# Performance work log

Measured on AMD Instinct MI355X. Metric: run time of the kernel, lower is better.

Reference implementation:

```python
import jax, jax.numpy as jnp
import numpy as np

HEADS = 12
HEAD_SIZE = 64
NEG_BIG = 1e12


def _rope_sin_cos(seq_len, head_size, dtype):
    # embeddings[n, 2i] = sin(n * 10000^(-2i/d)), [n, 2i+1] = cos(...)
    pos = jnp.arange(seq_len, dtype=dtype)                      # [s]
    idx = jnp.arange(head_size // 2, dtype=dtype)               # [d/2]
    inv_freq = jnp.power(jnp.asarray(10000.0, dtype), -2.0 * idx / head_size)
    ang = jnp.einsum('n,d->nd', pos, inv_freq)                  # [s, d/2]
    # cos_pos / sin_pos: repeat_interleave each frequency twice -> [1, s, 1, d]
    cos = jnp.repeat(jnp.cos(ang), 2, axis=-1)[None, :, None, :]
    sin = jnp.repeat(jnp.sin(ang), 2, axis=-1)[None, :, None, :]
    return sin, cos


def _rotate_half_interleaved(x):
    # stack([-x[..., 1::2], x[..., ::2]], -1).reshape_as(x)
    x2 = jnp.stack([-x[..., 1::2], x[..., ::2]], axis=-1)
    return x2.reshape(x.shape)


def setup_inputs() -> dict:
    key = jax.random.key(0)
    k1, k2 = jax.random.split(key)
    bs, s, h = 16, 512, 768
    hidden = jax.random.normal(k1, (bs, s, h), dtype=jnp.float32)
    attention_mask = jnp.ones((bs, s), dtype=jnp.int32)
    W = jax.random.normal(k2, (h, HEADS * 2 * HEAD_SIZE), dtype=jnp.float32) * (h ** -0.5)
    b = jnp.zeros((HEADS * 2 * HEAD_SIZE,), dtype=jnp.float32)
    return {"hidden": hidden, "attention_mask": attention_mask, "W": W, "b": b}


def reference(hidden, attention_mask, W, b):
    bs, s, _ = hidden.shape
    x = hidden @ W + b                                           # [b, s, heads*2*hd]
    x = x.reshape(bs, s, HEADS, 2, HEAD_SIZE)
    qw, kw = x[..., 0, :], x[..., 1, :]                          # [b, s, h, d]

    sin, cos = _rope_sin_cos(s, HEAD_SIZE, hidden.dtype)
    qw = qw * cos + _rotate_half_interleaved(qw) * sin
    kw = kw * cos + _rotate_half_interleaved(kw) * sin

    logits = jnp.einsum('bmhd,bnhd->bhmn', qw, kw)               # [b, h, s, s]

    am = attention_mask.astype(logits.dtype)
    pad_mask = 1.0 - am[:, None, None, :] * am[:, None, :, None]
    logits = logits - pad_mask * NEG_BIG

    tril = jnp.tril(jnp.ones((s, s), dtype=logits.dtype), k=-1)  # strictly lower
    logits = logits - tril[None, None, :, :] * NEG_BIG

    return logits / (HEAD_SIZE ** 0.5)
```

## Files before the change

### kernel.cpp

```cpp
#include <hip/hip_runtime.h>
#include <math.h>

#define HEADS 12
#define HSZ   64
#define SEQ   512
#define BATCH 16
#define HID   768
#define NOUT  1536
#define NEGQ  1.25e11f

typedef _Float16 f16x8 __attribute__((ext_vector_type(8)));
typedef _Float16 f16x4 __attribute__((ext_vector_type(4)));
typedef float    f32x4 __attribute__((ext_vector_type(4)));

__device__ __forceinline__ void async_ld16(const void* g, void* l) {
  __builtin_amdgcn_global_load_lds(
      (__attribute__((address_space(1))) void*)g,
      (__attribute__((address_space(3))) void*)l, 16, 0, 0);
}

__global__ __launch_bounds__(256) void prep_k(
    const float* __restrict__ hidden, const float* __restrict__ W,
    _Float16* __restrict__ Xb, _Float16* __restrict__ Wt,
    float2* __restrict__ tab)
{
  __shared__ float t_lds[32][33];
  const int b = blockIdx.x;
  const int t = threadIdx.x;
  if (b < 1152) {
    const int tk = b % 24, tn = b / 24;
    const int k0 = tk * 32, n0 = tn * 32;
    const int tx = t & 31, ty = t >> 5;
#pragma unroll
    for (int r = 0; r < 4; ++r)
      t_lds[ty + r * 8][tx] = W[(size_t)(k0 + ty + r * 8) * NOUT + n0 + tx];
    __syncthreads();
#pragma unroll
    for (int r = 0; r < 4; ++r)
      Wt[(size_t)(n0 + ty + r * 8) * HID + k0 + tx] = (_Float16)t_lds[tx][ty + r * 8];
  } else if (b < 1152 + 6144) {
    const int idx = (b - 1152) * 256 + t;
    float4 v = ((const float4*)hidden)[idx];
    f16x4 o;
    o.x = (_Float16)v.x; o.y = (_Float16)v.y;
    o.z = (_Float16)v.z; o.w = (_Float16)v.w;
    ((f16x4*)Xb)[idx] = o;
  } else {
    const int e = (b - 7296) * 256 + t;
    const int si = e >> 5, fi = e & 31;
    float inv = powf(10000.f, -(float)fi / 32.f);
    float ang = (float)si * inv;
    float sv, cv;
    sincosf(ang, &sv, &cv);
    tab[e] = make_float2(cv, sv);
  }
}

__global__ __launch_bounds__(256) void gemm1_k(
    const _Float16* __restrict__ Xb, const _Float16* __restrict__ Wt,
    const float* __restrict__ bias, const float2* __restrict__ tab,
    _Float16* __restrict__ qb, _Float16* __restrict__ kb)
{
  __shared__ __align__(16) _Float16 As[128 * 32];
  __shared__ __align__(16) _Float16 Bs[128 * 32];
  const int tid = threadIdx.x;
  const int lane = tid & 63;
  const int m0 = blockIdx.x * 128;
  const int n0 = blockIdx.y * 128;
  const int wm = ((tid >> 6) & 1) * 64;
  const int wn = (tid >> 7) * 64;

  const int s0r = tid >> 2, s0c = (tid & 3) * 8;
  const int s1r = (tid + 256) >> 2;
  const _Float16* ag0 = Xb + (size_t)(m0 + s0r) * HID + s0c;
  const _Float16* ag1 = Xb + (size_t)(m0 + s1r) * HID + s0c;
  const _Float16* bg0 = Wt + (size_t)(n0 + s0r) * HID + s0c;
  const _Float16* bg1 = Wt + (size_t)(n0 + s1r) * HID + s0c;
  _Float16* al0 = &As[tid * 8];
  _Float16* al1 = &As[(tid + 256) * 8];
  _Float16* bl0 = &Bs[tid * 8];
  _Float16* bl1 = &Bs[(tid + 256) * 8];

  const int lrow = lane & 15;
  const int lk = (lane >> 4) * 8;

  f32x4 acc[4][4] = {};

  for (int kt = 0; kt < 24; ++kt) {
    async_ld16(ag0, al0);
    async_ld16(ag1, al1);
    async_ld16(bg0, bl0);
    async_ld16(bg1, bl1);
    ag0 += 32; ag1 += 32; bg0 += 32; bg1 += 32;
    __syncthreads();
    f16x8 af[4], bf[4];
#pragma unroll
    for (int i = 0; i < 4; ++i) {
      af[i] = *(const f16x8*)&As[(wm + i * 16 + lrow) * 32 + lk];
      bf[i] = *(const f16x8*)&Bs[(wn + i * 16 + lrow) * 32 + lk];
    }
#pragma unroll
    for (int i = 0; i < 4; ++i)
#pragma unroll
      for (int j = 0; j < 4; ++j)
        acc[i][j] = __builtin_amdgcn_mfma_f32_16x16x32_f16(bf[j], af[i], acc[i][j], 0, 0, 0);
    __syncthreads();
  }

  const int qlane = lane >> 4;
  const int mlane = m0 + wm + (lane & 15);
#pragma unroll
  for (int j = 0; j < 4; ++j) {
    const int nb = n0 + wn + j * 16 + qlane * 4;
    const float4 b4 = *(const float4*)&bias[nb];
    const int d0 = nb & 63;
    const int h = nb >> 7;
    _Float16* dst = ((nb >> 6) & 1) ? kb : qb;
    const int fi0 = d0 >> 1;
#pragma unroll
    for (int i = 0; i < 4; ++i) {
      const int m = mlane + i * 16;
      const int si = m & (SEQ - 1);
      const int bb = m >> 9;
      const float4 cs = *(const float4*)&tab[si * 32 + fi0];
      const float v0 = acc[i][j][0] + b4.x;
      const float v1 = acc[i][j][1] + b4.y;
      const float v2 = acc[i][j][2] + b4.z;
      const float v3 = acc[i][j][3] + b4.w;
      f16x4 o;
      o.x = (_Float16)fmaf(v0, cs.x, -v1 * cs.y);
      o.y = (_Float16)fmaf(v1, cs.x, v0 * cs.y);
      o.z = (_Float16)fmaf(v2, cs.z, -v3 * cs.w);
      o.w = (_Float16)fmaf(v3, cs.z, v2 * cs.w);
      *(f16x4*)&dst[((size_t)(bb * HEADS + h) * SEQ + si) * HSZ + d0] = o;
    }
  }
}

__global__ __launch_bounds__(256) void gemm2_k(
    const _Float16* __restrict__ qb, const _Float16* __restrict__ kb,
    const int* __restrict__ am, float* __restrict__ out)
{
  __shared__ __align__(16) _Float16 Qs[2 * 128 * 32];
  __shared__ __align__(16) _Float16 Ks[2 * 128 * 32];
  const int tid = threadIdx.x;
  const int bh = blockIdx.y;
  const int bb = bh / HEADS;
  const int mt = blockIdx.x >> 2, nt = blockIdx.x & 3;
  const int m0 = mt * 128, n0 = nt * 128;
  const int* amb = am + bb * SEQ;
  float* obase = out + (size_t)bh * SEQ * SEQ;

  if (nt < mt) {
#pragma unroll
    for (int q = 0; q < 16; ++q) {
      const int f = q * 256 + tid;
      const int row = f >> 5, c4 = (f & 31) * 4;
      const int m = m0 + row;
      const float amm = (float)amb[m];
      const int nb = n0 + c4;
      const int4 a4 = *(const int4*)&amb[nb];
      float4 v;
      v.x = -(2.f - amm * (float)a4.x) * NEGQ;
      v.y = -(2.f - amm * (float)a4.y) * NEGQ;
      v.z = -(2.f - amm * (float)a4.z) * NEGQ;
      v.w = -(2.f - amm * (float)a4.w) * NEGQ;
      *(float4*)&obase[(size_t)m * SEQ + nb] = v;
    }
    return;
  }

  const _Float16* qg = qb + (size_t)bh * SEQ * HSZ;
  const _Float16* kg = kb + (size_t)bh * SEQ * HSZ;
#pragma unroll
  for (int ct = 0; ct < 4; ++ct) {
    const int s = ct * 256 + tid;
    const int half = s >> 9, row = (s >> 2) & 127, c8 = (s & 3) * 8;
    async_ld16(qg + (size_t)(m0 + row) * HSZ + half * 32 + c8, &Qs[s * 8]);
    async_ld16(kg + (size_t)(n0 + row) * HSZ + half * 32 + c8, &Ks[s * 8]);
  }
  __syncthreads();

  const int lane = tid & 63;
  const int wm = ((tid >> 6) & 1) * 64;
  const int wn = (tid >> 7) * 64;
  const int lrow = lane & 15;
  const int lk = (lane >> 4) * 8;
  f32x4 acc[4][4] = {};
#pragma unroll
  for (int half = 0; half < 2; ++half) {
    f16x8 af[4], bf[4];
#pragma unroll
    for (int i = 0; i < 4; ++i) {
      af[i] = *(const f16x8*)&Qs[half * 4096 + (wm + i * 16 + lrow) * 32 + lk];
      bf[i] = *(const f16x8*)&Ks[half * 4096 + (wn + i * 16 + lrow) * 32 + lk];
    }
#pragma unroll
    for (int i = 0; i < 4; ++i)
#pragma unroll
      for (int j = 0; j < 4; ++j)
        acc[i][j] = __builtin_amdgcn_mfma_f32_16x16x32_f16(bf[j], af[i], acc[i][j], 0, 0, 0);
  }

  const int qlane = lane >> 4;
  const int mlane = m0 + wm + (lane & 15);
#pragma unroll
  for (int i = 0; i < 4; ++i) {
    const int m = mlane + i * 16;
    const float amm = (float)amb[m];
    float* orow = obase + (size_t)m * SEQ;
#pragma unroll
    for (int j = 0; j < 4; ++j) {
      const int nb = n0 + wn + j * 16 + qlane * 4;
      const int4 a4 = *(const int4*)&amb[nb];
      float4 v;
      v.x = fmaf(acc[i][j][0], 0.125f,
                 -((float)(nb + 0 < m) + (1.f - amm * (float)a4.x)) * NEGQ);
      v.y = fmaf(acc[i][j][1], 0.125f,
                 -((float)(nb + 1 < m) + (1.f - amm * (float)a4.y)) * NEGQ);
      v.z = fmaf(acc[i][j][2], 0.125f,
                 -((float)(nb + 2 < m) + (1.f - amm * (float)a4.z)) * NEGQ);
      v.w = fmaf(acc[i][j][3], 0.125f,
                 -((float)(nb + 3 < m) + (1.f - amm * (float)a4.w)) * NEGQ);
      *(float4*)&orow[nb] = v;
    }
  }
}

extern "C" void kernel_launch(void* const* d_in, const int* in_sizes, int n_in,
                              void* d_out, int out_size, void* d_ws, size_t ws_size,
                              hipStream_t stream) {
  const float* hidden = (const float*)d_in[0];
  const int*   am     = (const int*)d_in[1];
  const float* W      = (const float*)d_in[2];
  const float* bias   = (const float*)d_in[3];
  float* out = (float*)d_out;
  char* ws = (char*)d_ws;
  _Float16* Xb = (_Float16*)(ws);
  _Float16* Wt = (_Float16*)(ws + 12582912);
  _Float16* qb = (_Float16*)(ws + 14942208);
  _Float16* kb = (_Float16*)(ws + 27525120);
  float2*   tab = (float2*)(ws + 40108032);

  prep_k<<<dim3(7360), dim3(256), 0, stream>>>(hidden, W, Xb, Wt, tab);
  gemm1_k<<<dim3(64, 12), dim3(256), 0, stream>>>(Xb, Wt, bias, tab, qb, kb);
  gemm2_k<<<dim3(16, 192), dim3(256), 0, stream>>>(qb, kb, am, out);
}
```

Before: 306.7 us.

## Quantize projection GEMM inputs to FP8 and use scaled MFMA with swizzled LDS

The hidden-state and weight conversion now packs values to FP8 instead of FP16. The first GEMM runs on the 16x16x128 FP8 scaled MFMA with 128-wide K tiles and an XOR-swizzled LDS layout, cutting conversion traffic and the number of K iterations. The Q·K kernel now loads operands straight from global memory into registers, and output stores become nontemporal. FP8 input precision loosens accuracy of the logits, which may push error tolerances.

After: 274.8 us. 1.12x faster.

```diff
diff --git a/kernel.cpp b/kernel.cpp
--- a/kernel.cpp
+++ b/kernel.cpp
@@ -4,7 +4,6 @@
 #define HEADS 12
 #define HSZ   64
 #define SEQ   512
-#define BATCH 16
 #define HID   768
 #define NOUT  1536
 #define NEGQ  1.25e11f
@@ -12,6 +11,8 @@
 typedef _Float16 f16x8 __attribute__((ext_vector_type(8)));
 typedef _Float16 f16x4 __attribute__((ext_vector_type(4)));
 typedef float    f32x4 __attribute__((ext_vector_type(4)));
+typedef int      i32x4 __attribute__((ext_vector_type(4)));
+typedef int      i32x8 __attribute__((ext_vector_type(8)));
 
 __device__ __forceinline__ void async_ld16(const void* g, void* l) {
   __builtin_amdgcn_global_load_lds(
@@ -21,7 +22,7 @@
 
 __global__ __launch_bounds__(256) void prep_k(
     const float* __restrict__ hidden, const float* __restrict__ W,
-    _Float16* __restrict__ Xb, _Float16* __restrict__ Wt,
+    unsigned char* __restrict__ Xb8, unsigned char* __restrict__ Wt8,
     float2* __restrict__ tab)
 {
   __shared__ float t_lds[32][33];
@@ -35,18 +36,28 @@
     for (int r = 0; r < 4; ++r)
       t_lds[ty + r * 8][tx] = W[(size_t)(k0 + ty + r * 8) * NOUT + n0 + tx];
     __syncthreads();
-#pragma unroll
-    for (int r = 0; r < 4; ++r)
-      Wt[(size_t)(n0 + ty + r * 8) * HID + k0 + tx] = (_Float16)t_lds[tx][ty + r * 8];
-  } else if (b < 1152 + 6144) {
+    const int nl = t >> 3, kg = t & 7;
+    int w = __builtin_amdgcn_cvt_pk_fp8_f32(t_lds[kg * 4 + 0][nl],
+                                            t_lds[kg * 4 + 1][nl], 0, false);
+    w = __builtin_amdgcn_cvt_pk_fp8_f32(t_lds[kg * 4 + 2][nl],
+                                        t_lds[kg * 4 + 3][nl], w, true);
+    *(int*)&Wt8[(size_t)(n0 + nl) * HID + k0 + kg * 4] = w;
+  } else if (b < 1152 + 1536) {
     const int idx = (b - 1152) * 256 + t;
-    float4 v = ((const float4*)hidden)[idx];
-    f16x4 o;
-    o.x = (_Float16)v.x; o.y = (_Float16)v.y;
-    o.z = (_Float16)v.z; o.w = (_Float16)v.w;
-    ((f16x4*)Xb)[idx] = o;
+    const float4* src = (const float4*)hidden + (size_t)idx * 4;
+    float4 v0 = src[0], v1 = src[1], v2 = src[2], v3 = src[3];
+    int4 o;
+    o.x = __builtin_amdgcn_cvt_pk_fp8_f32(v0.x, v0.y, 0, false);
+    o.x = __builtin_amdgcn_cvt_pk_fp8_f32(v0.z, v0.w, o.x, true);
+    o.y = __builtin_amdgcn_cvt_pk_fp8_f32(v1.x, v1.y, 0, false);
+    o.y = __builtin_amdgcn_cvt_pk_fp8_f32(v1.z, v1.w, o.y, true);
+    o.z = __builtin_amdgcn_cvt_pk_fp8_f32(v2.x, v2.y, 0, false);
+    o.z = __builtin_amdgcn_cvt_pk_fp8_f32(v2.z, v2.w, o.z, true);
+    o.w = __builtin_amdgcn_cvt_pk_fp8_f32(v3.x, v3.y, 0, false);
+    o.w = __builtin_amdgcn_cvt_pk_fp8_f32(v3.z, v3.w, o.w, true);
+    ((int4*)Xb8)[idx] = o;
   } else {
-    const int e = (b - 7296) * 256 + t;
+    const int e = (b - 2688) * 256 + t;
     const int si = e >> 5, fi = e & 31;
     float inv = powf(10000.f, -(float)fi / 32.f);
     float ang = (float)si * inv;
@@ -57,53 +68,55 @@
 }
 
 __global__ __launch_bounds__(256) void gemm1_k(
-    const _Float16* __restrict__ Xb, const _Float16* __restrict__ Wt,
+    const unsigned char* __restrict__ Xb8, const unsigned char* __restrict__ Wt8,
     const float* __restrict__ bias, const float2* __restrict__ tab,
     _Float16* __restrict__ qb, _Float16* __restrict__ kb)
 {
-  __shared__ __align__(16) _Float16 As[128 * 32];
-  __shared__ __align__(16) _Float16 Bs[128 * 32];
+  __shared__ __align__(16) int As4[4096];
+  __shared__ __align__(16) int Bs4[4096];
   const int tid = threadIdx.x;
   const int lane = tid & 63;
   const int m0 = blockIdx.x * 128;
   const int n0 = blockIdx.y * 128;
   const int wm = ((tid >> 6) & 1) * 64;
   const int wn = (tid >> 7) * 64;
-
-  const int s0r = tid >> 2, s0c = (tid & 3) * 8;
-  const int s1r = (tid + 256) >> 2;
-  const _Float16* ag0 = Xb + (size_t)(m0 + s0r) * HID + s0c;
-  const _Float16* ag1 = Xb + (size_t)(m0 + s1r) * HID + s0c;
-  const _Float16* bg0 = Wt + (size_t)(n0 + s0r) * HID + s0c;
-  const _Float16* bg1 = Wt + (size_t)(n0 + s1r) * HID + s0c;
-  _Float16* al0 = &As[tid * 8];
-  _Float16* al1 = &As[(tid + 256) * 8];
-  _Float16* bl0 = &Bs[tid * 8];
-  _Float16* bl1 = &Bs[(tid + 256) * 8];
-
   const int lrow = lane & 15;
-  const int lk = (lane >> 4) * 8;
+  const int q = lane >> 4;
 
   f32x4 acc[4][4] = {};
 
-  for (int kt = 0; kt < 24; ++kt) {
-    async_ld16(ag0, al0);
-    async_ld16(ag1, al1);
-    async_ld16(bg0, bl0);
-    async_ld16(bg1, bl1);
-    ag0 += 32; ag1 += 32; bg0 += 32; bg1 += 32;
+  for (int kt = 0; kt < 6; ++kt) {
+    const int kbase = kt * 128;
+#pragma unroll
+    for (int c = 0; c < 4; ++c) {
+      const int s = tid + c * 256;
+      const int row = s >> 3, cc = s & 7;
+      const int so = (((cc >> 1) ^ (row & 3)) << 5) + ((cc & 1) << 4);
+      async_ld16(Xb8 + (size_t)(m0 + row) * HID + kbase + so, (char*)As4 + s * 16);
+      async_ld16(Wt8 + (size_t)(n0 + row) * HID + kbase + so, (char*)Bs4 + s * 16);
+    }
     __syncthreads();
-    f16x8 af[4], bf[4];
+    i32x8 af[4], bf[4];
 #pragma unroll
     for (int i = 0; i < 4; ++i) {
-      af[i] = *(const f16x8*)&As[(wm + i * 16 + lrow) * 32 + lk];
-      bf[i] = *(const f16x8*)&Bs[(wn + i * 16 + lrow) * 32 + lk];
+      const int ra = wm + i * 16 + lrow;
+      const int oa = ra * 32 + ((q ^ (ra & 3)) << 3);
+      i32x4 lo = *(const i32x4*)&As4[oa];
+      i32x4 hi = *(const i32x4*)&As4[oa + 4];
+      af[i] = (i32x8){lo.x, lo.y, lo.z, lo.w, hi.x, hi.y, hi.z, hi.w};
+      const int rb = wn + i * 16 + lrow;
+      const int ob = rb * 32 + ((q ^ (rb & 3)) << 3);
+      lo = *(const i32x4*)&Bs4[ob];
+      hi = *(const i32x4*)&Bs4[ob + 4];
+      bf[i] = (i32x8){lo.x, lo.y, lo.z, lo.w, hi.x, hi.y, hi.z, hi.w};
     }
 #pragma unroll
     for (int i = 0; i < 4; ++i)
 #pragma unroll
       for (int j = 0; j < 4; ++j)
-        acc[i][j] = __builtin_amdgcn_mfma_f32_16x16x32_f16(bf[j], af[i], acc[i][j], 0, 0, 0);
+        acc[i][j] = __builtin_amdgcn_mfma_scale_f32_16x16x128_f8f6f4(
+            bf[j], af[i], acc[i][j], 0, 0,
+            0, 0x7F7F7F7F, 0, 0x7F7F7F7F);
     __syncthreads();
   }
 
@@ -141,8 +154,6 @@
     const _Float16* __restrict__ qb, const _Float16* __restrict__ kb,
     const int* __restrict__ am, float* __restrict__ out)
 {
-  __shared__ __align__(16) _Float16 Qs[2 * 128 * 32];
-  __shared__ __align__(16) _Float16 Ks[2 * 128 * 32];
   const int tid = threadIdx.x;
   const int bh = blockIdx.y;
   const int bb = bh / HEADS;
@@ -153,54 +164,48 @@
 
   if (nt < mt) {
 #pragma unroll
-    for (int q = 0; q < 16; ++q) {
-      const int f = q * 256 + tid;
+    for (int p = 0; p < 16; ++p) {
+      const int f = p * 256 + tid;
       const int row = f >> 5, c4 = (f & 31) * 4;
       const int m = m0 + row;
       const float amm = (float)amb[m];
       const int nb = n0 + c4;
       const int4 a4 = *(const int4*)&amb[nb];
-      float4 v;
-      v.x = -(2.f - amm * (float)a4.x) * NEGQ;
-      v.y = -(2.f - amm * (float)a4.y) * NEGQ;
-      v.z = -(2.f - amm * (float)a4.z) * NEGQ;
-      v.w = -(2.f - amm * (float)a4.w) * NEGQ;
-      *(float4*)&obase[(size_t)m * SEQ + nb] = v;
+      f32x4 v;
+      v[0] = -(2.f - amm * (float)a4.x) * NEGQ;
+      v[1] = -(2.f - amm * (float)a4.y) * NEGQ;
+      v[2] = -(2.f - amm * (float)a4.z) * NEGQ;
+      v[3] = -(2.f - amm * (float)a4.w) * NEGQ;
+      __builtin_nontemporal_store(v, (f32x4*)&obase[(size_t)m * SEQ + nb]);
     }
     return;
   }
 
   const _Float16* qg = qb + (size_t)bh * SEQ * HSZ;
   const _Float16* kg = kb + (size_t)bh * SEQ * HSZ;
-#pragma unroll
-  for (int ct = 0; ct < 4; ++ct) {
-    const int s = ct * 256 + tid;
-    const int half = s >> 9, row = (s >> 2) & 127, c8 = (s & 3) * 8;
-    async_ld16(qg + (size_t)(m0 + row) * HSZ + half * 32 + c8, &Qs[s * 8]);
-    async_ld16(kg + (size_t)(n0 + row) * HSZ + half * 32 + c8, &Ks[s * 8]);
-  }
-  __syncthreads();
-
   const int lane = tid & 63;
   const int wm = ((tid >> 6) & 1) * 64;
   const int wn = (tid >> 7) * 64;
   const int lrow = lane & 15;
   const int lk = (lane >> 4) * 8;
+
+  f16x8 af[4][2], bf[4][2];
+#pragma unroll
+  for (int i = 0; i < 4; ++i)
+#pragma unroll
+    for (int h = 0; h < 2; ++h) {
+      af[i][h] = *(const f16x8*)(qg + (size_t)(m0 + wm + i * 16 + lrow) * HSZ + h * 32 + lk);
+      bf[i][h] = *(const f16x8*)(kg + (size_t)(n0 + wn + i * 16 + lrow) * HSZ + h * 32 + lk);
+    }
+
   f32x4 acc[4][4] = {};
 #pragma unroll
-  for (int half = 0; half < 2; ++half) {
-    f16x8 af[4], bf[4];
-#pragma unroll
-    for (int i = 0; i < 4; ++i) {
-      af[i] = *(const f16x8*)&Qs[half * 4096 + (wm + i * 16 + lrow) * 32 + lk];
-      bf[i] = *(const f16x8*)&Ks[half * 4096 + (wn + i * 16 + lrow) * 32 + lk];
-    }
+  for (int h = 0; h < 2; ++h)
 #pragma unroll
     for (int i = 0; i < 4; ++i)
 #pragma unroll
       for (int j = 0; j < 4; ++j)
-        acc[i][j] = __builtin_amdgcn_mfma_f32_16x16x32_f16(bf[j], af[i], acc[i][j], 0, 0, 0);
-  }
+        acc[i][j] = __builtin_amdgcn_mfma_f32_16x16x32_f16(bf[j][h], af[i][h], acc[i][j], 0, 0, 0);
 
   const int qlane = lane >> 4;
   const int mlane = m0 + wm + (lane & 15);
@@ -213,16 +218,16 @@
     for (int j = 0; j < 4; ++j) {
       const int nb = n0 + wn + j * 16 + qlane * 4;
       const int4 a4 = *(const int4*)&amb[nb];
-      float4 v;
-      v.x = fmaf(acc[i][j][0], 0.125f,
-                 -((float)(nb + 0 < m) + (1.f - amm * (float)a4.x)) * NEGQ);
-      v.y = fmaf(acc[i][j][1], 0.125f,
-                 -((float)(nb + 1 < m) + (1.f - amm * (float)a4.y)) * NEGQ);
-      v.z = fmaf(acc[i][j][2], 0.125f,
-                 -((float)(nb + 2 < m) + (1.f - amm * (float)a4.z)) * NEGQ);
-      v.w = fmaf(acc[i][j][3], 0.125f,
-                 -((float)(nb + 3 < m) + (1.f - amm * (float)a4.w)) * NEGQ);
-      *(float4*)&orow[nb] = v;
+      f32x4 v;
+      v[0] = fmaf(acc[i][j][0], 0.125f,
+                  -((float)(nb + 0 < m) + (1.f - amm * (float)a4.x)) * NEGQ);
+      v[1] = fmaf(acc[i][j][1], 0.125f,
+                  -((float)(nb + 1 < m) + (1.f - amm * (float)a4.y)) * NEGQ);
+      v[2] = fmaf(acc[i][j][2], 0.125f,
+                  -((float)(nb + 2 < m) + (1.f - amm * (float)a4.z)) * NEGQ);
+      v[3] = fmaf(acc[i][j][3], 0.125f,
+                  -((float)(nb + 3 < m) + (1.f - amm * (float)a4.w)) * NEGQ);
+      __builtin_nontemporal_store(v, (f32x4*)&orow[nb]);
     }
   }
 }
@@ -236,13 +241,13 @@
   const float* bias   = (const float*)d_in[3];
   float* out = (float*)d_out;
   char* ws = (char*)d_ws;
-  _Float16* Xb = (_Float16*)(ws);
-  _Float16* Wt = (_Float16*)(ws + 12582912);
-  _Float16* qb = (_Float16*)(ws + 14942208);
-  _Float16* kb = (_Float16*)(ws + 27525120);
-  float2*   tab = (float2*)(ws + 40108032);
-
-  prep_k<<<dim3(7360), dim3(256), 0, stream>>>(hidden, W, Xb, Wt, tab);
-  gemm1_k<<<dim3(64, 12), dim3(256), 0, stream>>>(Xb, Wt, bias, tab, qb, kb);
+  unsigned char* Xb8 = (unsigned char*)(ws);
+  unsigned char* Wt8 = (unsigned char*)(ws + 6291456);
+  _Float16* qb = (_Float16*)(ws + 7471104);
+  _Float16* kb = (_Float16*)(ws + 20054016);
+  float2*   tab = (float2*)(ws + 32636928);
+
+  prep_k<<<dim3(2752), dim3(256), 0, stream>>>(hidden, W, Xb8, Wt8, tab);
+  gemm1_k<<<dim3(64, 12), dim3(256), 0, stream>>>(Xb8, Wt8, bias, tab, qb, kb);
   gemm2_k<<<dim3(16, 192), dim3(256), 0, stream>>>(qb, kb, am, out);
 }
```
